# Optimization experiments

Hardware: AMD Instinct MI355X
Metric: run time of the kernel (lower is better)

The kernel has to match this reference:

```python
import jax, jax.numpy as jnp
import numpy as np

N_NODES = 128   # input_series_dim (nodes per graph)
FEAT = 512      # input_series_length
HID = 512       # hidden_channels
OUT = 10        # output_dimension
BATCH = 512     # batch_size


def setup_inputs() -> dict:
    key = jax.random.key(0)
    ks = jax.random.split(key, 9)
    s = 0.02
    x = jax.random.normal(ks[0], (BATCH, N_NODES, FEAT), jnp.float32)
    # dense_to_sparse(ones(N_NODES, N_NODES)) -> fully connected incl. diagonal,
    # row-major order, covering only nodes 0..N_NODES-1 (faithful to source).
    r = jnp.repeat(jnp.arange(N_NODES, dtype=jnp.int32), N_NODES)
    c = jnp.tile(jnp.arange(N_NODES, dtype=jnp.int32), N_NODES)
    edge_index = jnp.stack([r, c])  # (2, N_NODES**2)
    batch = jnp.repeat(jnp.arange(BATCH, dtype=jnp.int32), N_NODES)  # (BATCH*N_NODES,)
    W1 = jax.random.normal(ks[1], (FEAT, HID), jnp.float32) * s
    b1 = jnp.zeros((HID,), jnp.float32)
    W2 = jax.random.normal(ks[2], (HID, HID), jnp.float32) * s
    b2 = jnp.zeros((HID,), jnp.float32)
    W3 = jax.random.normal(ks[3], (HID, HID), jnp.float32) * s
    b3 = jnp.zeros((HID,), jnp.float32)
    Wlin = jax.random.normal(ks[4], (HID, OUT), jnp.float32) * s
    blin = jnp.zeros((OUT,), jnp.float32)
    return {"x": x, "W1": W1, "b1": b1, "W2": W2, "b2": b2, "W3": W3,
            "b3": b3, "Wlin": Wlin, "blin": blin,
            "edge_index": edge_index, "batch": batch}


def gcn_conv(h, src, dst, W, b):
    # PyG GCNConv: linear transform, add self-loops for ALL N nodes, symmetric norm,
    # scatter-add aggregate at dst, add bias.
    N = h.shape[0]
    h = h @ W
    loop = jnp.arange(N, dtype=src.dtype)
    s = jnp.concatenate([src, loop])
    d = jnp.concatenate([dst, loop])
    deg = jax.ops.segment_sum(jnp.ones(s.shape[0], h.dtype), d, num_segments=N)
    dinv = jnp.where(deg > 0, jax.lax.rsqrt(deg), jnp.zeros((), h.dtype))
    norm = dinv[s] * dinv[d]                     # (E+N,)
    out = jax.ops.segment_sum(norm[:, None] * h[s], d, num_segments=N)
    return out + b


def reference(x, W1, b1, W2, b2, W3, b3, Wlin, blin, edge_index, batch):
    x = x.reshape(-1, x.shape[-1]).astype(jnp.float32)   # (B*N_NODES, FEAT)
    src, dst = edge_index[0], edge_index[1]
    h = jax.nn.relu(gcn_conv(x, src, dst, W1, b1))
    h = jax.nn.relu(gcn_conv(h, src, dst, W2, b2))
    h = gcn_conv(h, src, dst, W3, b3)                    # layers == 3 path
    B = BATCH
    sums = jax.ops.segment_sum(h, batch, num_segments=B)
    cnt = jax.ops.segment_sum(jnp.ones((h.shape[0],), h.dtype), batch, num_segments=B)
    pooled = sums / cnt[:, None]                         # global_mean_pool
    # dropout p=0.5 is identity in eval mode
    return pooled @ Wlin + blin                          # (BATCH, OUT)
```

## Files before the change

kernel.cpp:

```cpp
#include <hip/hip_runtime.h>
#include <hip/hip_bf16.h>


typedef __attribute__((ext_vector_type(8))) short short8;
typedef __attribute__((ext_vector_type(4))) float f32x4;
typedef __attribute__((ext_vector_type(2))) unsigned int uint2v;

#define AS_G __attribute__((address_space(1)))
#define AS_L __attribute__((address_space(3)))

__device__ __forceinline__ void gload_lds16(const void* g, void* l) {
  __builtin_amdgcn_global_load_lds((const AS_G void*)g, (AS_L void*)l, 16, 0, 0);
}

__device__ __forceinline__ unsigned int pack2_bf16(float a, float b) {
  unsigned int ua = __float_as_uint(a);
  unsigned int ub = __float_as_uint(b);
  ua += 0x7FFFu + ((ua >> 16) & 1u);
  ub += 0x7FFFu + ((ub >> 16) & 1u);
  return (ua >> 16) | (ub & 0xFFFF0000u);
}

__device__ __forceinline__ unsigned short bf16_rne(float a) {
  unsigned int ua = __float_as_uint(a);
  ua += 0x7FFFu + ((ua >> 16) & 1u);
  return (unsigned short)(ua >> 16);
}

__global__ __launch_bounds__(512, 4) void gemm1(
    const unsigned short* __restrict__ xb,
    const __hip_bfloat16* __restrict__ W1t,
    const float* __restrict__ b1,
    unsigned short* __restrict__ H1)
{
  __shared__ __align__(16) __hip_bfloat16 smem[26368];

  const int t    = threadIdx.x;
  const int orig = blockIdx.x;
  const int wgid = (orig & 7) * 128 + (orig >> 3);
  const int g    = wgid >> 1;
  const int nb   = wgid & 1;

  const int wave = t >> 6;
  const int l    = t & 63;
  const int q    = l >> 4;
  const int r16  = l & 15;
  const int wm   = (wave & 1) * 64;
  const int wn   = (wave >> 1) * 64;

  const int arow = t >> 2;
  const int slot = t & 3;
  const unsigned short* gaA = xb + (size_t)(g * 128 + arow) * 512 +
                              ((slot ^ ((arow >> 1) & 3)) << 3);
  const int nrow0 = t >> 2;
  const int nrow1 = 128 + (t >> 2);
  const __hip_bfloat16* gb0 = W1t + (size_t)(nb * 256 + nrow0) * 512 +
                              ((slot ^ ((nrow0 >> 1) & 3)) << 3);
  const __hip_bfloat16* gb1 = W1t + (size_t)(nb * 256 + nrow1) * 512 +
                              ((slot ^ ((nrow1 >> 1) & 3)) << 3);

  f32x4 acc[4][4];
#pragma unroll
  for (int i = 0; i < 4; ++i)
#pragma unroll
    for (int j = 0; j < 4; ++j)
      acc[i][j] = (f32x4)0.0f;

  gload_lds16(gaA, smem + wave * 512);
  gload_lds16(gb0, smem + 8192 + wave * 512);
  gload_lds16(gb1, smem + 8192 + 4096 + wave * 512);

  for (int kt = 0; kt < 16; ++kt) {
    const int cur = kt & 1;
    const int nxt = cur ^ 1;
    __syncthreads();

    if (kt < 15) {
      const int ko = (kt + 1) * 32;
      gload_lds16(gaA + ko, smem + nxt * 4096 + wave * 512);
      gload_lds16(gb0 + ko, smem + 8192 + nxt * 8192 + wave * 512);
      gload_lds16(gb1 + ko, smem + 8192 + nxt * 8192 + 4096 + wave * 512);
    }

    short8 af[4], bfr[4];
#pragma unroll
    for (int i = 0; i < 4; ++i) {
      const int row = wm + i * 16 + r16;
      const int c   = (q ^ ((row >> 1) & 3)) << 3;
      af[i] = *(const short8*)(const void*)(smem + cur * 4096 + row * 32 + c);
    }
#pragma unroll
    for (int j = 0; j < 4; ++j) {
      const int row = wn + j * 16 + r16;
      const int c   = (q ^ ((row >> 1) & 3)) << 3;
      bfr[j] = *(const short8*)(const void*)(smem + 8192 + cur * 8192 + row * 32 + c);
    }
    __builtin_amdgcn_s_setprio(1);
#pragma unroll
    for (int i = 0; i < 4; ++i)
#pragma unroll
      for (int j = 0; j < 4; ++j)
        acc[i][j] = __builtin_amdgcn_mfma_f32_16x16x32_bf16(af[i], bfr[j], acc[i][j], 0, 0, 0);
    __builtin_amdgcn_s_setprio(0);
  }

  float* redf = (float*)(smem + 24576);
  float* Sbuf = (float*)(smem + 25600);
  const size_t hbase = (size_t)g * 128 * 512 + nb * 256;

  if (g == 0) {
    float sj[4];
#pragma unroll
    for (int j = 0; j < 4; ++j) {
      float a = 0.0f;
#pragma unroll
      for (int i = 0; i < 4; ++i)
#pragma unroll
        for (int r = 0; r < 4; ++r)
          a += acc[i][j][r];
      a += __shfl_xor(a, 16, 64);
      a += __shfl_xor(a, 32, 64);
      sj[j] = a;
    }
    __syncthreads();
    if (q == 0) {
#pragma unroll
      for (int j = 0; j < 4; ++j) redf[wave * 64 + j * 16 + r16] = sj[j];
    }
    __syncthreads();
    if (t < 256)
      Sbuf[t] = redf[(2 * (t >> 6)) * 64 + (t & 63)] +
                redf[(2 * (t >> 6) + 1) * 64 + (t & 63)];
    __syncthreads();
    float bvv[4], Svv[4];
#pragma unroll
    for (int j = 0; j < 4; ++j) {
      bvv[j] = b1[nb * 256 + wn + j * 16 + r16];
      Svv[j] = Sbuf[wn + j * 16 + r16];
    }
#pragma unroll
    for (int i = 0; i < 4; ++i)
#pragma unroll
      for (int r = 0; r < 4; ++r) {
        const int row = wm + i * 16 + q * 4 + r;
#pragma unroll
        for (int j = 0; j < 4; ++j) {
          const float v = fmaxf((Svv[j] + acc[i][j][r]) * (1.0f / 129.0f) + bvv[j], 0.0f);
          const float o = __shfl_xor(v, 1, 64);
          if ((r16 & 1) == 0)
            *(unsigned int*)(void*)(H1 + hbase + (size_t)row * 512 + wn + j * 16 + r16) =
                pack2_bf16(v, o);
        }
      }
  } else {
    float bvv[4];
#pragma unroll
    for (int j = 0; j < 4; ++j) bvv[j] = b1[nb * 256 + wn + j * 16 + r16];
#pragma unroll
    for (int i = 0; i < 4; ++i)
#pragma unroll
      for (int r = 0; r < 4; ++r) {
        const int row = wm + i * 16 + q * 4 + r;
#pragma unroll
        for (int j = 0; j < 4; ++j) {
          const float v = fmaxf(acc[i][j][r] + bvv[j], 0.0f);
          const float o = __shfl_xor(v, 1, 64);
          if ((r16 & 1) == 0)
            *(unsigned int*)(void*)(H1 + hbase + (size_t)row * 512 + wn + j * 16 + r16) =
                pack2_bf16(v, o);
        }
      }
  }
}

__global__ __launch_bounds__(512, 4) void gemm2(
    const unsigned short* __restrict__ H1,
    const __hip_bfloat16* __restrict__ W2t,
    const float* __restrict__ b2,
    float* __restrict__ P)
{
  __shared__ __align__(16) __hip_bfloat16 smem[26368];

  const int t    = threadIdx.x;
  const int orig = blockIdx.x;
  const int wgid = (orig & 7) * 128 + (orig >> 3);
  const int g    = wgid >> 1;
  const int nb   = wgid & 1;

  const int wave = t >> 6;
  const int l    = t & 63;
  const int q    = l >> 4;
  const int r16  = l & 15;
  const int wm   = (wave & 1) * 64;
  const int wn   = (wave >> 1) * 64;

  const int arow = t >> 2;
  const int slot = t & 3;
  const unsigned short* gaA = H1 + (size_t)(g * 128 + arow) * 512 +
                              ((slot ^ ((arow >> 1) & 3)) << 3);
  const int nrow0 = t >> 2;
  const int nrow1 = 128 + (t >> 2);
  const __hip_bfloat16* gb0 = W2t + (size_t)(nb * 256 + nrow0) * 512 +
                              ((slot ^ ((nrow0 >> 1) & 3)) << 3);
  const __hip_bfloat16* gb1 = W2t + (size_t)(nb * 256 + nrow1) * 512 +
                              ((slot ^ ((nrow1 >> 1) & 3)) << 3);

  f32x4 acc[4][4];
#pragma unroll
  for (int i = 0; i < 4; ++i)
#pragma unroll
    for (int j = 0; j < 4; ++j)
      acc[i][j] = (f32x4)0.0f;

  gload_lds16(gaA, smem + wave * 512);
  gload_lds16(gb0, smem + 8192 + wave * 512);
  gload_lds16(gb1, smem + 8192 + 4096 + wave * 512);

  for (int kt = 0; kt < 16; ++kt) {
    const int cur = kt & 1;
    const int nxt = cur ^ 1;
    __syncthreads();

    if (kt < 15) {
      const int ko = (kt + 1) * 32;
      gload_lds16(gaA + ko, smem + nxt * 4096 + wave * 512);
      gload_lds16(gb0 + ko, smem + 8192 + nxt * 8192 + wave * 512);
      gload_lds16(gb1 + ko, smem + 8192 + nxt * 8192 + 4096 + wave * 512);
    }

    short8 af[4], bfr[4];
#pragma unroll
    for (int i = 0; i < 4; ++i) {
      const int row = wm + i * 16 + r16;
      const int c   = (q ^ ((row >> 1) & 3)) << 3;
      af[i] = *(const short8*)(const void*)(smem + cur * 4096 + row * 32 + c);
    }
#pragma unroll
    for (int j = 0; j < 4; ++j) {
      const int row = wn + j * 16 + r16;
      const int c   = (q ^ ((row >> 1) & 3)) << 3;
      bfr[j] = *(const short8*)(const void*)(smem + 8192 + cur * 8192 + row * 32 + c);
    }
    __builtin_amdgcn_s_setprio(1);
#pragma unroll
    for (int i = 0; i < 4; ++i)
#pragma unroll
      for (int j = 0; j < 4; ++j)
        acc[i][j] = __builtin_amdgcn_mfma_f32_16x16x32_bf16(af[i], bfr[j], acc[i][j], 0, 0, 0);
    __builtin_amdgcn_s_setprio(0);
  }

  float* redf = (float*)(smem + 24576);
  float* Sbuf = (float*)(smem + 25600);

  float pj[4];
  if (g == 0) {
    float sj[4];
#pragma unroll
    for (int j = 0; j < 4; ++j) {
      float a = 0.0f;
#pragma unroll
      for (int i = 0; i < 4; ++i)
#pragma unroll
        for (int r = 0; r < 4; ++r)
          a += acc[i][j][r];
      a += __shfl_xor(a, 16, 64);
      a += __shfl_xor(a, 32, 64);
      sj[j] = a;
    }
    __syncthreads();
    if (q == 0) {
#pragma unroll
      for (int j = 0; j < 4; ++j) redf[wave * 64 + j * 16 + r16] = sj[j];
    }
    __syncthreads();
    if (t < 256)
      Sbuf[t] = redf[(2 * (t >> 6)) * 64 + (t & 63)] +
                redf[(2 * (t >> 6) + 1) * 64 + (t & 63)];
    __syncthreads();
#pragma unroll
    for (int j = 0; j < 4; ++j) {
      const int col = wn + j * 16 + r16;
      const float bv = b2[nb * 256 + col];
      const float Sv = Sbuf[col];
      float a = 0.0f;
#pragma unroll
      for (int i = 0; i < 4; ++i)
#pragma unroll
        for (int r = 0; r < 4; ++r)
          a += fmaxf((Sv + acc[i][j][r]) * (1.0f / 129.0f) + bv, 0.0f);
      a += __shfl_xor(a, 16, 64);
      a += __shfl_xor(a, 32, 64);
      pj[j] = a;
    }
    __syncthreads();
  } else {
#pragma unroll
    for (int j = 0; j < 4; ++j) {
      const float bv = b2[nb * 256 + wn + j * 16 + r16];
      float a = 0.0f;
#pragma unroll
      for (int i = 0; i < 4; ++i)
#pragma unroll
        for (int r = 0; r < 4; ++r)
          a += fmaxf(acc[i][j][r] + bv, 0.0f);
      a += __shfl_xor(a, 16, 64);
      a += __shfl_xor(a, 32, 64);
      pj[j] = a;
    }
    __syncthreads();
  }
  if (q == 0) {
#pragma unroll
    for (int j = 0; j < 4; ++j) redf[wave * 64 + j * 16 + r16] = pj[j];
  }
  __syncthreads();
  if (t < 256)
    P[(size_t)g * 512 + nb * 256 + t] =
        (redf[(2 * (t >> 6)) * 64 + (t & 63)] +
         redf[(2 * (t >> 6) + 1) * 64 + (t & 63)]) * (1.0f / 128.0f);
}

__global__ void final_out(const float* __restrict__ P,
                          const float* __restrict__ Wf,
                          const float* __restrict__ bfv,
                          float* __restrict__ out) {
  const int m = blockIdx.x;
  const int l = threadIdx.x;
  float acc[10];
#pragma unroll
  for (int o = 0; o < 10; ++o) acc[o] = 0.0f;
  for (int c = l; c < 512; c += 64) {
    const float p = P[m * 512 + c];
#pragma unroll
    for (int o = 0; o < 10; ++o) acc[o] += p * Wf[c * 10 + o];
  }
#pragma unroll
  for (int off = 32; off; off >>= 1)
#pragma unroll
    for (int o = 0; o < 10; ++o) acc[o] += __shfl_down(acc[o], off, 64);
  if (l == 0) {
#pragma unroll
    for (int o = 0; o < 10; ++o) out[m * 10 + o] = acc[o] + bfv[o];
  }
}

__global__ __launch_bounds__(1024) void fused_gcn(
    const float* __restrict__ x,
    const __hip_bfloat16* __restrict__ W1t,
    const __hip_bfloat16* __restrict__ W2t,
    const float* __restrict__ b1,
    const float* __restrict__ b2,
    const float* __restrict__ Wf,
    const float* __restrict__ bfv,
    float* __restrict__ out)
{
  __shared__ __align__(16) __hip_bfloat16 smem[81920];

  const int t  = threadIdx.x;
  const int g  = blockIdx.x;
  const int wave = t >> 6;
  const int l    = t & 63;
  const int q    = l >> 4;
  const int r16  = l & 15;
  const int wm   = (wave & 1) * 64;
  const int wn   = (wave >> 1) * 64;

  const int arow = t >> 3;
  const int kq   = t & 7;
  const float* ga = x + ((size_t)g * 128 + arow) * 512 + kq * 4;
  const int awoff = arow * 32 + (((kq >> 1) ^ ((arow >> 1) & 3)) << 3) + (kq & 1) * 4;

  const int brow = t >> 2;
  const int bgc  = (t & 3) ^ ((brow >> 1) & 3);
  const size_t boff = (size_t)brow * 512 + bgc * 8;
  const __hip_bfloat16* g1b0 = W1t + boff;
  const __hip_bfloat16* g1b1 = g1b0 + (size_t)256 * 512;

  f32x4 acc[4][4];
#pragma unroll
  for (int i = 0; i < 4; ++i)
#pragma unroll
    for (int j = 0; j < 4; ++j)
      acc[i][j] = (f32x4)0.0f;

  {
    f32x4 a0 = *(const f32x4*)(const void*)ga;
    gload_lds16(g1b0, smem + 49152 + wave * 512);
    gload_lds16(g1b1, smem + 49152 + 8192 + wave * 512);
    uint2v w;
    w[0] = pack2_bf16(a0[0], a0[1]);
    w[1] = pack2_bf16(a0[2], a0[3]);
    *(uint2v*)(void*)(smem + awoff) = w;
  }
  for (int kt = 0; kt < 16; ++kt) {
    const int cur = kt & 1;
    const int nxt = cur ^ 1;
    __syncthreads();

    f32x4 aN;
    if (kt < 15) {
      const int ko = (kt + 1) * 32;
      aN = *(const f32x4*)(const void*)(ga + ko);
      gload_lds16(g1b0 + ko, smem + 49152 + nxt * 16384 + wave * 512);
      gload_lds16(g1b1 + ko, smem + 49152 + nxt * 16384 + 8192 + wave * 512);
    }

    short8 af[4], bfr[4];
#pragma unroll
    for (int i = 0; i < 4; ++i) {
      const int row = wm + i * 16 + r16;
      const int c   = (q ^ ((row >> 1) & 3)) << 3;
      af[i] = *(const short8*)(const void*)(smem + cur * 4096 + row * 32 + c);
    }
#pragma unroll
    for (int j = 0; j < 4; ++j) {
      const int row = wn + j * 16 + r16;
      const int c   = (q ^ ((row >> 1) & 3)) << 3;
      bfr[j] = *(const short8*)(const void*)(smem + 49152 + cur * 16384 + row * 32 + c);
    }
#pragma unroll
    for (int i = 0; i < 4; ++i)
#pragma unroll
      for (int j = 0; j < 4; ++j)
        acc[i][j] = __builtin_amdgcn_mfma_f32_16x16x32_bf16(af[i], bfr[j], acc[i][j], 0, 0, 0);

    if (kt < 15) {
      uint2v w;
      w[0] = pack2_bf16(aN[0], aN[1]);
      w[1] = pack2_bf16(aN[2], aN[3]);
      *(uint2v*)(void*)(smem + nxt * 4096 + awoff) = w;
    }
  }
  __syncthreads();

  const __hip_bfloat16* g2b0 = W2t + boff;
  const __hip_bfloat16* g2b1 = g2b0 + (size_t)256 * 512;
  gload_lds16(g2b0, smem + 65536 + wave * 512);

  float* redf = (float*)(smem + 73728);
  float* Sbuf = (float*)(smem + 75776);

  if (g == 0) {
    float sj[4];
#pragma unroll
    for (int j = 0; j < 4; ++j) {
      float a = 0.0f;
#pragma unroll
      for (int i = 0; i < 4; ++i)
#pragma unroll
        for (int r = 0; r < 4; ++r)
          a += acc[i][j][r];
      a += __shfl_xor(a, 16, 64);
      a += __shfl_xor(a, 32, 64);
      sj[j] = a;
    }
    if (q == 0) {
#pragma unroll
      for (int j = 0; j < 4; ++j) redf[wave * 64 + j * 16 + r16] = sj[j];
    }
    __syncthreads();
    if (t < 512)
      Sbuf[t] = redf[((t >> 6) * 2) * 64 + (t & 63)] +
                redf[((t >> 6) * 2 + 1) * 64 + (t & 63)];
    __syncthreads();
#pragma unroll
    for (int j = 0; j < 4; ++j) {
      const int col = wn + j * 16 + r16;
      const float bv = b1[col];
      const float Sv = Sbuf[col];
#pragma unroll
      for (int i = 0; i < 4; ++i)
#pragma unroll
        for (int r = 0; r < 4; ++r) {
          const int row = wm + i * 16 + q * 4 + r;
          const float v = fmaxf((Sv + acc[i][j][r]) * (1.0f / 129.0f) + bv, 0.0f);
          const float o = __shfl_xor(v, 1, 64);
          if ((r16 & 1) == 0) {
            const int sl = (col >> 3) ^ (row & 7);
            *(unsigned int*)(void*)(smem + row * 512 + sl * 8 + (col & 7)) = pack2_bf16(v, o);
          }
        }
    }
  } else {
#pragma unroll
    for (int j = 0; j < 4; ++j) {
      const int col = wn + j * 16 + r16;
      const float bv = b1[col];
#pragma unroll
      for (int i = 0; i < 4; ++i)
#pragma unroll
        for (int r = 0; r < 4; ++r) {
          const int row = wm + i * 16 + q * 4 + r;
          const float v = fmaxf(acc[i][j][r] + bv, 0.0f);
          const float o = __shfl_xor(v, 1, 64);
          if ((r16 & 1) == 0) {
            const int sl = (col >> 3) ^ (row & 7);
            *(unsigned int*)(void*)(smem + row * 512 + sl * 8 + (col & 7)) = pack2_bf16(v, o);
          }
        }
    }
  }

#pragma unroll
  for (int i = 0; i < 4; ++i)
#pragma unroll
    for (int j = 0; j < 4; ++j)
      acc[i][j] = (f32x4)0.0f;

  for (int kt = 0; kt < 16; ++kt) {
    __syncthreads();
    gload_lds16(g2b1 + kt * 32, smem + 73728 + wave * 512);
    if (wave < 8) {
      short8 af[4], bfr[4];
#pragma unroll
      for (int i = 0; i < 4; ++i) {
        const int row = wm + i * 16 + r16;
        const int sl  = (kt * 4 + q) ^ (row & 7);
        af[i] = *(const short8*)(const void*)(smem + row * 512 + sl * 8);
      }
#pragma unroll
      for (int j = 0; j < 4; ++j) {
        const int row = wn + j * 16 + r16;
        const int c   = (q ^ ((row >> 1) & 3)) << 3;
        bfr[j] = *(const short8*)(const void*)(smem + 65536 + row * 32 + c);
      }
      __builtin_amdgcn_s_setprio(1);
#pragma unroll
      for (int i = 0; i < 4; ++i)
#pragma unroll
        for (int j = 0; j < 4; ++j)
          acc[i][j] = __builtin_amdgcn_mfma_f32_16x16x32_bf16(af[i], bfr[j], acc[i][j], 0, 0, 0);
      __builtin_amdgcn_s_setprio(0);
    }
    __syncthreads();
    if (kt < 15)
      gload_lds16(g2b0 + (kt + 1) * 32, smem + 65536 + wave * 512);
    if (wave >= 8) {
      short8 af[4], bfr[4];
#pragma unroll
      for (int i = 0; i < 4; ++i) {
        const int row = wm + i * 16 + r16;
        const int sl  = (kt * 4 + q) ^ (row & 7);
        af[i] = *(const short8*)(const void*)(smem + row * 512 + sl * 8);
      }
#pragma unroll
      for (int j = 0; j < 4; ++j) {
        const int row = wn + j * 16 + r16;
        const int c   = (q ^ ((row >> 1) & 3)) << 3;
        bfr[j] = *(const short8*)(const void*)(smem + 65536 + row * 32 + c);
      }
      __builtin_amdgcn_s_setprio(1);
#pragma unroll
      for (int i = 0; i < 4; ++i)
#pragma unroll
        for (int j = 0; j < 4; ++j)
          acc[i][j] = __builtin_amdgcn_mfma_f32_16x16x32_bf16(af[i], bfr[j], acc[i][j], 0, 0, 0);
      __builtin_amdgcn_s_setprio(0);
    }
  }
  __syncthreads();

  float pj[4];
  if (g == 0) {
    float sj[4];
#pragma unroll
    for (int j = 0; j < 4; ++j) {
      float a = 0.0f;
#pragma unroll
      for (int i = 0; i < 4; ++i)
#pragma unroll
        for (int r = 0; r < 4; ++r)
          a += acc[i][j][r];
      a += __shfl_xor(a, 16, 64);
      a += __shfl_xor(a, 32, 64);
      sj[j] = a;
    }
    if (q == 0) {
#pragma unroll
      for (int j = 0; j < 4; ++j) redf[wave * 64 + j * 16 + r16] = sj[j];
    }
    __syncthreads();
    if (t < 512)
      Sbuf[t] = redf[((t >> 6) * 2) * 64 + (t & 63)] +
                redf[((t >> 6) * 2 + 1) * 64 + (t & 63)];
    __syncthreads();
#pragma unroll
    for (int j = 0; j < 4; ++j) {
      const float bv = b2[wn + j * 16 + r16];
      const float Sv = Sbuf[wn + j * 16 + r16];
      float a = 0.0f;
#pragma unroll
      for (int i = 0; i < 4; ++i)
#pragma unroll
        for (int r = 0; r < 4; ++r)
          a += fmaxf((Sv + acc[i][j][r]) * (1.0f / 129.0f) + bv, 0.0f);
      a += __shfl_xor(a, 16, 64);
      a += __shfl_xor(a, 32, 64);
      pj[j] = a;
    }
  } else {
#pragma unroll
    for (int j = 0; j < 4; ++j) {
      const float bv = b2[wn + j * 16 + r16];
      float a = 0.0f;
#pragma unroll
      for (int i = 0; i < 4; ++i)
#pragma unroll
        for (int r = 0; r < 4; ++r)
          a += fmaxf(acc[i][j][r] + bv, 0.0f);
      a += __shfl_xor(a, 16, 64);
      a += __shfl_xor(a, 32, 64);
      pj[j] = a;
    }
  }
  if (q == 0) {
#pragma unroll
    for (int j = 0; j < 4; ++j) redf[wave * 64 + j * 16 + r16] = pj[j];
  }
  __syncthreads();
  if (t < 512)
    Sbuf[t] =
        (redf[((t >> 6) * 2) * 64 + (t & 63)] +
         redf[((t >> 6) * 2 + 1) * 64 + (t & 63)]) * (1.0f / 128.0f);
  __syncthreads();

  if (wave < 10) {
    float s = 0.0f;
    for (int c = l; c < 512; c += 64) s += Sbuf[c] * Wf[c * 10 + wave];
#pragma unroll
    for (int off = 32; off; off >>= 1) s += __shfl_down(s, off, 64);
    if (l == 0) out[(size_t)g * 10 + wave] = s + bfv[wave];
  }
}

__global__ __launch_bounds__(1024) void prep(
    const float* __restrict__ W1, const float* __restrict__ W2,
    unsigned short* __restrict__ W1t, unsigned short* __restrict__ W2t,
    const float* __restrict__ W3, const float* __restrict__ Wlin,
    const float* __restrict__ b3, const float* __restrict__ blin,
    float* __restrict__ Wf, float* __restrict__ bfv,
    const float* __restrict__ x, unsigned short* __restrict__ xb) {
  const int b = blockIdx.x;
  if (b < 512) {
    __shared__ float tile[32][33];
    const int z  = b >> 8;
    const int by = (b >> 4) & 15;
    const int bx = b & 15;
    const float* W = z ? W2 : W1;
    unsigned short* Wt = z ? W2t : W1t;
    const int tx = threadIdx.x & 31;
    const int ty = threadIdx.x >> 5;
    tile[ty][tx] = W[(by * 32 + ty) * 512 + bx * 32 + tx];
    __syncthreads();
    Wt[(bx * 32 + ty) * 512 + by * 32 + tx] = bf16_rne(tile[tx][ty]);
  } else if (b < 1024) {
    const int c = b - 512;
    const int l = threadIdx.x;
    if (l < 64) {
      float acc[10];
#pragma unroll
      for (int o = 0; o < 10; ++o) acc[o] = 0.0f;
      for (int n = l; n < 512; n += 64) {
        const float wv = W3[c * 512 + n];
#pragma unroll
        for (int o = 0; o < 10; ++o) acc[o] += wv * Wlin[n * 10 + o];
      }
#pragma unroll
      for (int off = 32; off; off >>= 1)
#pragma unroll
        for (int o = 0; o < 10; ++o) acc[o] += __shfl_down(acc[o], off, 64);
      if (l == 0) {
#pragma unroll
        for (int o = 0; o < 10; ++o) Wf[c * 10 + o] = acc[o];
      }
      if (c < 10) {
        float s = 0.0f;
        for (int k = l; k < 512; k += 64) s += b3[k] * Wlin[k * 10 + c];
#pragma unroll
        for (int off = 32; off; off >>= 1) s += __shfl_down(s, off, 64);
        if (l == 0) bfv[c] = s + blin[c];
      }
    }
  } else {
    const size_t base = (size_t)(b - 1024) * 8192;
    const int tt = threadIdx.x;
#pragma unroll
    for (int jj = 0; jj < 2; ++jj) {
      const size_t off = base + (size_t)jj * 4096 + (size_t)tt * 4;
      const f32x4 v = *(const f32x4*)(const void*)(x + off);
      uint2v w;
      w[0] = pack2_bf16(v[0], v[1]);
      w[1] = pack2_bf16(v[2], v[3]);
      *(uint2v*)(void*)(xb + off) = w;
    }
  }
}

extern "C" void kernel_launch(void* const* d_in, const int* in_sizes, int n_in,
                              void* d_out, int out_size, void* d_ws, size_t ws_size,
                              hipStream_t stream) {
  const float* x    = (const float*)d_in[0];
  const float* W1   = (const float*)d_in[1];
  const float* b1   = (const float*)d_in[2];
  const float* W2   = (const float*)d_in[3];
  const float* b2   = (const float*)d_in[4];
  const float* W3   = (const float*)d_in[5];
  const float* b3   = (const float*)d_in[6];
  const float* Wlin = (const float*)d_in[7];
  const float* blin = (const float*)d_in[8];
  float* out = (float*)d_out;

  char* ws = (char*)d_ws;
  unsigned short* W1t = (unsigned short*)ws;
  unsigned short* W2t = W1t + 512 * 512;
  float* Wf           = (float*)(W2t + 512 * 512);
  float* bfv          = Wf + 512 * 10;
  float* P            = bfv + 16;
  unsigned short* H1  = (unsigned short*)(P + 512 * 512);
  unsigned short* xb  = H1 + (size_t)65536 * 512;

  const size_t need = (size_t)512 * 512 * 2 * 2 +
                      (512 * 10 + 16 + 512 * 512) * 4 +
                      (size_t)65536 * 512 * 2 * 2;

  const bool split = ws_size >= need;

  prep<<<split ? 5120 : 1024, 1024, 0, stream>>>(
      W1, W2, W1t, W2t, W3, Wlin, b3, blin, Wf, bfv, x, xb);

  if (split) {
    gemm1<<<1024, 512, 0, stream>>>(xb, (const __hip_bfloat16*)W1t, b1, H1);
    gemm2<<<1024, 512, 0, stream>>>(H1, (const __hip_bfloat16*)W2t, b2, P);
    final_out<<<512, 64, 0, stream>>>(P, Wf, bfv, out);
  } else {
    fused_gcn<<<512, 1024, 0, stream>>>(
        x, (const __hip_bfloat16*)W1t, (const __hip_bfloat16*)W2t, b1, b2, Wf, bfv, out);
  }
}
```

Measured before the change: 297.2 us.

## Load weight B-fragments directly from global into registers, bypassing LDS

Result: slower. 366.8 us (+23.4%).

```diff
diff --git a/kernel.cpp b/kernel.cpp
--- a/kernel.cpp
+++ b/kernel.cpp
@@ -33,7 +33,7 @@
     const float* __restrict__ b1,
     unsigned short* __restrict__ H1)
 {
-  __shared__ __align__(16) __hip_bfloat16 smem[26368];
+  __shared__ __align__(16) __hip_bfloat16 smem[9728];
 
   const int t    = threadIdx.x;
   const int orig = blockIdx.x;
@@ -52,12 +52,8 @@
   const int slot = t & 3;
   const unsigned short* gaA = xb + (size_t)(g * 128 + arow) * 512 +
                               ((slot ^ ((arow >> 1) & 3)) << 3);
-  const int nrow0 = t >> 2;
-  const int nrow1 = 128 + (t >> 2);
-  const __hip_bfloat16* gb0 = W1t + (size_t)(nb * 256 + nrow0) * 512 +
-                              ((slot ^ ((nrow0 >> 1) & 3)) << 3);
-  const __hip_bfloat16* gb1 = W1t + (size_t)(nb * 256 + nrow1) * 512 +
-                              ((slot ^ ((nrow1 >> 1) & 3)) << 3);
+
+  const int bvo = (nb * 256 + wn + r16) * 512 + q * 8;
 
   f32x4 acc[4][4];
 #pragma unroll
@@ -67,34 +63,27 @@
       acc[i][j] = (f32x4)0.0f;
 
   gload_lds16(gaA, smem + wave * 512);
-  gload_lds16(gb0, smem + 8192 + wave * 512);
-  gload_lds16(gb1, smem + 8192 + 4096 + wave * 512);
 
   for (int kt = 0; kt < 16; ++kt) {
     const int cur = kt & 1;
     const int nxt = cur ^ 1;
     __syncthreads();
 
-    if (kt < 15) {
-      const int ko = (kt + 1) * 32;
-      gload_lds16(gaA + ko, smem + nxt * 4096 + wave * 512);
-      gload_lds16(gb0 + ko, smem + 8192 + nxt * 8192 + wave * 512);
-      gload_lds16(gb1 + ko, smem + 8192 + nxt * 8192 + 4096 + wave * 512);
-    }
-
-    short8 af[4], bfr[4];
+    short8 bfr[4];
+#pragma unroll
+    for (int j = 0; j < 4; ++j)
+      bfr[j] = *(const short8*)(const void*)(W1t + bvo + j * 8192 + kt * 32);
+
+    if (kt < 15)
+      gload_lds16(gaA + (kt + 1) * 32, smem + nxt * 4096 + wave * 512);
+
+    short8 af[4];
 #pragma unroll
     for (int i = 0; i < 4; ++i) {
       const int row = wm + i * 16 + r16;
       const int c   = (q ^ ((row >> 1) & 3)) << 3;
       af[i] = *(const short8*)(const void*)(smem + cur * 4096 + row * 32 + c);
     }
-#pragma unroll
-    for (int j = 0; j < 4; ++j) {
-      const int row = wn + j * 16 + r16;
-      const int c   = (q ^ ((row >> 1) & 3)) << 3;
-      bfr[j] = *(const short8*)(const void*)(smem + 8192 + cur * 8192 + row * 32 + c);
-    }
     __builtin_amdgcn_s_setprio(1);
 #pragma unroll
     for (int i = 0; i < 4; ++i)
@@ -104,8 +93,8 @@
     __builtin_amdgcn_s_setprio(0);
   }
 
-  float* redf = (float*)(smem + 24576);
-  float* Sbuf = (float*)(smem + 25600);
+  float* redf = (float*)(smem + 8192);
+  float* Sbuf = (float*)(smem + 9216);
   const size_t hbase = (size_t)g * 128 * 512 + nb * 256;
 
   if (g == 0) {
@@ -179,7 +168,7 @@
     const float* __restrict__ b2,
     float* __restrict__ P)
 {
-  __shared__ __align__(16) __hip_bfloat16 smem[26368];
+  __shared__ __align__(16) __hip_bfloat16 smem[9728];
 
   const int t    = threadIdx.x;
   const int orig = blockIdx.x;
@@ -198,12 +187,8 @@
   const int slot = t & 3;
   const unsigned short* gaA = H1 + (size_t)(g * 128 + arow) * 512 +
                               ((slot ^ ((arow >> 1) & 3)) << 3);
-  const int nrow0 = t >> 2;
-  const int nrow1 = 128 + (t >> 2);
-  const __hip_bfloat16* gb0 = W2t + (size_t)(nb * 256 + nrow0) * 512 +
-                              ((slot ^ ((nrow0 >> 1) & 3)) << 3);
-  const __hip_bfloat16* gb1 = W2t + (size_t)(nb * 256 + nrow1) * 512 +
-                              ((slot ^ ((nrow1 >> 1) & 3)) << 3);
+
+  const int bvo = (nb * 256 + wn + r16) * 512 + q * 8;
 
   f32x4 acc[4][4];
 #pragma unroll
@@ -213,34 +198,27 @@
       acc[i][j] = (f32x4)0.0f;
 
   gload_lds16(gaA, smem + wave * 512);
-  gload_lds16(gb0, smem + 8192 + wave * 512);
-  gload_lds16(gb1, smem + 8192 + 4096 + wave * 512);
 
   for (int kt = 0; kt < 16; ++kt) {
     const int cur = kt & 1;
     const int nxt = cur ^ 1;
     __syncthreads();
 
-    if (kt < 15) {
-      const int ko = (kt + 1) * 32;
-      gload_lds16(gaA + ko, smem + nxt * 4096 + wave * 512);
-      gload_lds16(gb0 + ko, smem + 8192 + nxt * 8192 + wave * 512);
-      gload_lds16(gb1 + ko, smem + 8192 + nxt * 8192 + 4096 + wave * 512);
-    }
-
-    short8 af[4], bfr[4];
+    short8 bfr[4];
+#pragma unroll
+    for (int j = 0; j < 4; ++j)
+      bfr[j] = *(const short8*)(const void*)(W2t + bvo + j * 8192 + kt * 32);
+
+    if (kt < 15)
+      gload_lds16(gaA + (kt + 1) * 32, smem + nxt * 4096 + wave * 512);
+
+    short8 af[4];
 #pragma unroll
     for (int i = 0; i < 4; ++i) {
       const int row = wm + i * 16 + r16;
       const int c   = (q ^ ((row >> 1) & 3)) << 3;
       af[i] = *(const short8*)(const void*)(smem + cur * 4096 + row * 32 + c);
     }
-#pragma unroll
-    for (int j = 0; j < 4; ++j) {
-      const int row = wn + j * 16 + r16;
-      const int c   = (q ^ ((row >> 1) & 3)) << 3;
-      bfr[j] = *(const short8*)(const void*)(smem + 8192 + cur * 8192 + row * 32 + c);
-    }
     __builtin_amdgcn_s_setprio(1);
 #pragma unroll
     for (int i = 0; i < 4; ++i)
@@ -250,8 +228,8 @@
     __builtin_amdgcn_s_setprio(0);
   }
 
-  float* redf = (float*)(smem + 24576);
-  float* Sbuf = (float*)(smem + 25600);
+  float* redf = (float*)(smem + 8192);
+  float* Sbuf = (float*)(smem + 9216);
 
   float pj[4];
   if (g == 0) {
```

## Fuse fp32-to-bf16 conversion of x into gemm1 and triple-buffer LDS pipelines

Applied to the files above, without the earlier changes.

Result: no change. 294.3 us (-1.0%).

```diff
diff --git a/kernel.cpp b/kernel.cpp
--- a/kernel.cpp
+++ b/kernel.cpp
@@ -5,6 +5,7 @@
 typedef __attribute__((ext_vector_type(8))) short short8;
 typedef __attribute__((ext_vector_type(4))) float f32x4;
 typedef __attribute__((ext_vector_type(2))) unsigned int uint2v;
+typedef __attribute__((ext_vector_type(4))) unsigned int uint4v;
 
 #define AS_G __attribute__((address_space(1)))
 #define AS_L __attribute__((address_space(3)))
@@ -12,6 +13,13 @@
 __device__ __forceinline__ void gload_lds16(const void* g, void* l) {
   __builtin_amdgcn_global_load_lds((const AS_G void*)g, (AS_L void*)l, 16, 0, 0);
 }
+
+#define FENCE_BARRIER()                      \
+  do {                                       \
+    asm volatile("" ::: "memory");           \
+    __builtin_amdgcn_s_barrier();            \
+    asm volatile("" ::: "memory");           \
+  } while (0)
 
 __device__ __forceinline__ unsigned int pack2_bf16(float a, float b) {
   unsigned int ua = __float_as_uint(a);
@@ -28,12 +36,12 @@
 }
 
 __global__ __launch_bounds__(512, 4) void gemm1(
-    const unsigned short* __restrict__ xb,
+    const float* __restrict__ x,
     const __hip_bfloat16* __restrict__ W1t,
     const float* __restrict__ b1,
     unsigned short* __restrict__ H1)
 {
-  __shared__ __align__(16) __hip_bfloat16 smem[26368];
+  __shared__ __align__(16) __hip_bfloat16 smem[38400];
 
   const int t    = threadIdx.x;
   const int orig = blockIdx.x;
@@ -50,8 +58,9 @@
 
   const int arow = t >> 2;
   const int slot = t & 3;
-  const unsigned short* gaA = xb + (size_t)(g * 128 + arow) * 512 +
-                              ((slot ^ ((arow >> 1) & 3)) << 3);
+  const int achk = slot ^ ((arow >> 1) & 3);
+  const float* gx = x + (size_t)(g * 128 + arow) * 512 + achk * 8;
+
   const int nrow0 = t >> 2;
   const int nrow1 = 128 + (t >> 2);
   const __hip_bfloat16* gb0 = W1t + (size_t)(nb * 256 + nrow0) * 512 +
@@ -66,34 +75,60 @@
     for (int j = 0; j < 4; ++j)
       acc[i][j] = (f32x4)0.0f;
 
-  gload_lds16(gaA, smem + wave * 512);
-  gload_lds16(gb0, smem + 8192 + wave * 512);
-  gload_lds16(gb1, smem + 8192 + 4096 + wave * 512);
+  int u0 = 0, u1 = 12288, u2 = 24576;
+
+  f32x4 pA0, pA1;
+  pA0 = *(const f32x4*)(const void*)gx;
+  pA1 = *(const f32x4*)(const void*)(gx + 4);
+  gload_lds16(gb0, smem + u0 + 4096 + wave * 512);
+  gload_lds16(gb1, smem + u0 + 8192 + wave * 512);
+  {
+    uint4v w;
+    w[0] = pack2_bf16(pA0[0], pA0[1]);
+    w[1] = pack2_bf16(pA0[2], pA0[3]);
+    w[2] = pack2_bf16(pA1[0], pA1[1]);
+    w[3] = pack2_bf16(pA1[2], pA1[3]);
+    *(uint4v*)(void*)(smem + u0 + t * 8) = w;
+  }
+  pA0 = *(const f32x4*)(const void*)(gx + 32);
+  pA1 = *(const f32x4*)(const void*)(gx + 36);
+  gload_lds16(gb0 + 32, smem + u1 + 4096 + wave * 512);
+  gload_lds16(gb1 + 32, smem + u1 + 8192 + wave * 512);
+  asm volatile("s_waitcnt vmcnt(4)" ::: "memory");
+  asm volatile("s_waitcnt lgkmcnt(0)" ::: "memory");
+  FENCE_BARRIER();
 
   for (int kt = 0; kt < 16; ++kt) {
-    const int cur = kt & 1;
-    const int nxt = cur ^ 1;
-    __syncthreads();
-
     if (kt < 15) {
-      const int ko = (kt + 1) * 32;
-      gload_lds16(gaA + ko, smem + nxt * 4096 + wave * 512);
-      gload_lds16(gb0 + ko, smem + 8192 + nxt * 8192 + wave * 512);
-      gload_lds16(gb1 + ko, smem + 8192 + nxt * 8192 + 4096 + wave * 512);
-    }
-
+      uint4v w;
+      w[0] = pack2_bf16(pA0[0], pA0[1]);
+      w[1] = pack2_bf16(pA0[2], pA0[3]);
+      w[2] = pack2_bf16(pA1[0], pA1[1]);
+      w[3] = pack2_bf16(pA1[2], pA1[3]);
+      *(uint4v*)(void*)(smem + u1 + t * 8) = w;
+    }
+    if (kt < 14) {
+      const int ko = (kt + 2) * 32;
+      pA0 = *(const f32x4*)(const void*)(gx + ko);
+      pA1 = *(const f32x4*)(const void*)(gx + ko + 4);
+      gload_lds16(gb0 + ko, smem + u2 + 4096 + wave * 512);
+      gload_lds16(gb1 + ko, smem + u2 + 8192 + wave * 512);
+      asm volatile("s_waitcnt vmcnt(4)" ::: "memory");
+    } else {
+      asm volatile("s_waitcnt vmcnt(0)" ::: "memory");
+    }
     short8 af[4], bfr[4];
 #pragma unroll
     for (int i = 0; i < 4; ++i) {
       const int row = wm + i * 16 + r16;
       const int c   = (q ^ ((row >> 1) & 3)) << 3;
-      af[i] = *(const short8*)(const void*)(smem + cur * 4096 + row * 32 + c);
+      af[i] = *(const short8*)(const void*)(smem + u0 + row * 32 + c);
     }
 #pragma unroll
     for (int j = 0; j < 4; ++j) {
       const int row = wn + j * 16 + r16;
       const int c   = (q ^ ((row >> 1) & 3)) << 3;
-      bfr[j] = *(const short8*)(const void*)(smem + 8192 + cur * 8192 + row * 32 + c);
+      bfr[j] = *(const short8*)(const void*)(smem + u0 + 4096 + row * 32 + c);
     }
     __builtin_amdgcn_s_setprio(1);
 #pragma unroll
@@ -102,10 +137,17 @@
       for (int j = 0; j < 4; ++j)
         acc[i][j] = __builtin_amdgcn_mfma_f32_16x16x32_bf16(af[i], bfr[j], acc[i][j], 0, 0, 0);
     __builtin_amdgcn_s_setprio(0);
-  }
-
-  float* redf = (float*)(smem + 24576);
-  float* Sbuf = (float*)(smem + 25600);
+
+    if (kt < 15) {
+      asm volatile("s_waitcnt lgkmcnt(0)" ::: "memory");
+      FENCE_BARRIER();
+    }
+    const int tmp = u0; u0 = u1; u1 = u2; u2 = tmp;
+  }
+  __syncthreads();
+
+  float* redf = (float*)(smem + 36864);
+  float* Sbuf = (float*)(smem + 37888);
   const size_t hbase = (size_t)g * 128 * 512 + nb * 256;
 
   if (g == 0) {
@@ -179,7 +221,7 @@
     const float* __restrict__ b2,
     float* __restrict__ P)
 {
-  __shared__ __align__(16) __hip_bfloat16 smem[26368];
+  __shared__ __align__(16) __hip_bfloat16 smem[38400];
 
   const int t    = threadIdx.x;
   const int orig = blockIdx.x;
@@ -212,34 +254,39 @@
     for (int j = 0; j < 4; ++j)
       acc[i][j] = (f32x4)0.0f;
 
-  gload_lds16(gaA, smem + wave * 512);
-  gload_lds16(gb0, smem + 8192 + wave * 512);
-  gload_lds16(gb1, smem + 8192 + 4096 + wave * 512);
+  int u0 = 0, u1 = 12288, u2 = 24576;
+
+  gload_lds16(gaA,      smem + u0 + wave * 512);
+  gload_lds16(gb0,      smem + u0 + 4096 + wave * 512);
+  gload_lds16(gb1,      smem + u0 + 8192 + wave * 512);
+  gload_lds16(gaA + 32, smem + u1 + wave * 512);
+  gload_lds16(gb0 + 32, smem + u1 + 4096 + wave * 512);
+  gload_lds16(gb1 + 32, smem + u1 + 8192 + wave * 512);
+  asm volatile("s_waitcnt vmcnt(3)" ::: "memory");
+  FENCE_BARRIER();
 
   for (int kt = 0; kt < 16; ++kt) {
-    const int cur = kt & 1;
-    const int nxt = cur ^ 1;
-    __syncthreads();
-
-    if (kt < 15) {
-      const int ko = (kt + 1) * 32;
-      gload_lds16(gaA + ko, smem + nxt * 4096 + wave * 512);
-      gload_lds16(gb0 + ko, smem + 8192 + nxt * 8192 + wave * 512);
-      gload_lds16(gb1 + ko, smem + 8192 + nxt * 8192 + 4096 + wave * 512);
-    }
-
+    if (kt < 14) {
+      const int ko = (kt + 2) * 32;
+      gload_lds16(gaA + ko, smem + u2 + wave * 512);
+      gload_lds16(gb0 + ko, smem + u2 + 4096 + wave * 512);
+      gload_lds16(gb1 + ko, smem + u2 + 8192 + wave * 512);
+      asm volatile("s_waitcnt vmcnt(3)" ::: "memory");
+    } else {
+      asm volatile("s_waitcnt vmcnt(0)" ::: "memory");
+    }
     short8 af[4], bfr[4];
 #pragma unroll
     for (int i = 0; i < 4; ++i) {
       const int row = wm + i * 16 + r16;
       const int c   = (q ^ ((row >> 1) & 3)) << 3;
-      af[i] = *(const short8*)(const void*)(smem + cur * 4096 + row * 32 + c);
+      af[i] = *(const short8*)(const void*)(smem + u0 + row * 32 + c);
     }
 #pragma unroll
     for (int j = 0; j < 4; ++j) {
       const int row = wn + j * 16 + r16;
       const int c   = (q ^ ((row >> 1) & 3)) << 3;
-      bfr[j] = *(const short8*)(const void*)(smem + 8192 + cur * 8192 + row * 32 + c);
+      bfr[j] = *(const short8*)(const void*)(smem + u0 + 4096 + row * 32 + c);
     }
     __builtin_amdgcn_s_setprio(1);
 #pragma unroll
@@ -248,10 +295,17 @@
       for (int j = 0; j < 4; ++j)
         acc[i][j] = __builtin_amdgcn_mfma_f32_16x16x32_bf16(af[i], bfr[j], acc[i][j], 0, 0, 0);
     __builtin_amdgcn_s_setprio(0);
-  }
-
-  float* redf = (float*)(smem + 24576);
-  float* Sbuf = (float*)(smem + 25600);
+
+    if (kt < 15) {
+      asm volatile("s_waitcnt lgkmcnt(0)" ::: "memory");
+      FENCE_BARRIER();
+    }
+    const int tmp = u0; u0 = u1; u1 = u2; u2 = tmp;
+  }
+  __syncthreads();
+
+  float* redf = (float*)(smem + 36864);
+  float* Sbuf = (float*)(smem + 37888);
 
   float pj[4];
   if (g == 0) {
@@ -639,8 +693,7 @@
     unsigned short* __restrict__ W1t, unsigned short* __restrict__ W2t,
     const float* __restrict__ W3, const float* __restrict__ Wlin,
     const float* __restrict__ b3, const float* __restrict__ blin,
-    float* __restrict__ Wf, float* __restrict__ bfv,
-    const float* __restrict__ x, unsigned short* __restrict__ xb) {
+    float* __restrict__ Wf, float* __restrict__ bfv) {
   const int b = blockIdx.x;
   if (b < 512) {
     __shared__ float tile[32][33];
@@ -654,7 +707,7 @@
     tile[ty][tx] = W[(by * 32 + ty) * 512 + bx * 32 + tx];
     __syncthreads();
     Wt[(bx * 32 + ty) * 512 + by * 32 + tx] = bf16_rne(tile[tx][ty]);
-  } else if (b < 1024) {
+  } else {
     const int c = b - 512;
     const int l = threadIdx.x;
     if (l < 64) {
@@ -681,18 +734,6 @@
         for (int off = 32; off; off >>= 1) s += __shfl_down(s, off, 64);
         if (l == 0) bfv[c] = s + blin[c];
       }
-    }
-  } else {
-    const size_t base = (size_t)(b - 1024) * 8192;
-    const int tt = threadIdx.x;
-#pragma unroll
-    for (int jj = 0; jj < 2; ++jj) {
-      const size_t off = base + (size_t)jj * 4096 + (size_t)tt * 4;
-      const f32x4 v = *(const f32x4*)(const void*)(x + off);
-      uint2v w;
-      w[0] = pack2_bf16(v[0], v[1]);
-      w[1] = pack2_bf16(v[2], v[3]);
-      *(uint2v*)(void*)(xb + off) = w;
     }
   }
 }
@@ -718,19 +759,18 @@
   float* bfv          = Wf + 512 * 10;
   float* P            = bfv + 16;
   unsigned short* H1  = (unsigned short*)(P + 512 * 512);
-  unsigned short* xb  = H1 + (size_t)65536 * 512;
 
   const size_t need = (size_t)512 * 512 * 2 * 2 +
                       (512 * 10 + 16 + 512 * 512) * 4 +
-                      (size_t)65536 * 512 * 2 * 2;
+                      (size_t)65536 * 512 * 2;
 
   const bool split = ws_size >= need;
 
-  prep<<<split ? 5120 : 1024, 1024, 0, stream>>>(
-      W1, W2, W1t, W2t, W3, Wlin, b3, blin, Wf, bfv, x, xb);
+  prep<<<1024, 1024, 0, stream>>>(
+      W1, W2, W1t, W2t, W3, Wlin, b3, blin, Wf, bfv);
 
   if (split) {
-    gemm1<<<1024, 512, 0, stream>>>(xb, (const __hip_bfloat16*)W1t, b1, H1);
+    gemm1<<<1024, 512, 0, stream>>>(x, (const __hip_bfloat16*)W1t, b1, H1);
     gemm2<<<1024, 512, 0, stream>>>(H1, (const __hip_bfloat16*)W2t, b2, P);
     final_out<<<512, 64, 0, stream>>>(P, Wf, bfv, out);
   } else {
```
